# Kernel optimization log

Hardware: AMD Instinct MI355X
Metric: run time of the kernel (lower is better)

The kernel has to match this reference:

```python
import jax, jax.numpy as jnp
import numpy as np

GAMMA = 0.96875


def setup_inputs() -> dict:
    key = jax.random.key(0)
    kx, kq, kk, kv = jax.random.split(key, 4)
    B, T, D = 4, 2048, 1024
    x = jax.random.normal(kx, (B, T, D), dtype=jnp.float32)
    Wq = jax.random.normal(kq, (D, D), dtype=jnp.float32) * (1.0 / np.sqrt(D))
    Wk = jax.random.normal(kk, (D, D), dtype=jnp.float32) * (1.0 / np.sqrt(D))
    Wv = jax.random.normal(kv, (D, D), dtype=jnp.float32) * (1.0 / np.sqrt(D))
    return {"x": x, "Wq": Wq, "Wk": Wk, "Wv": Wv}


def reference(x, Wq, Wk, Wv):
    # x: [B, T, D_in]; projections are bias-free Dense layers
    B, T, _ = x.shape
    D = Wq.shape[1]
    Q = jnp.einsum("bti,id->btd", x, Wq)  # [B,T,D]
    K = jnp.einsum("bti,id->btd", x, Wk)
    V = jnp.einsum("bti,id->btd", x, Wv)

    gamma = jnp.asarray(GAMMA, x.dtype)

    # Original: s[t] = gamma*s[t-1] + K[:,t,:]^T @ V[:,t,:]   (a [D,D] state,
    # batch is CONTRACTED by the matmul), then only reduce_sum over the last
    # state axis is used. The recurrence is linear, so it collapses exactly to
    # a [D]-vector recurrence with m_t[d] = sum_b K[b,t,d] * (sum_e V[b,t,e]).
    m = jnp.einsum("btd,bt->td", K, V.sum(axis=-1))  # [T,D]

    def step(s, mt):
        s_new = gamma * s + mt
        return s_new, s_new

    # loop runs t = 1..T-1 starting from s = 0; afterwards s[0] = s[1]
    _, states = jax.lax.scan(step, jnp.zeros((D,), x.dtype), m[1:])  # [T-1,D]
    S = jnp.concatenate([states[:1], states], axis=0)  # [T,D]

    # tf.reshape([T,D] -> [-1, T]) is a row-major element scramble, then transpose
    S = S.reshape(-1, T).T  # [T,D] (scrambled, faithful to the original)

    return S[None, :, :] * Q  # broadcast over batch -> [B,T,D]
```

## Files before the change

### kernel.cpp

```cpp
#include <hip/hip_runtime.h>
#include <hip/hip_bf16.h>
#include <cstddef>

#define T_DIM 2048
#define D_DIM 1024
#define GAMMA_F 0.96875f

typedef __attribute__((ext_vector_type(8))) short bf16x8;
typedef __attribute__((ext_vector_type(4))) ushort ushortx4;
typedef __attribute__((ext_vector_type(8))) ushort ushortx8;
typedef __attribute__((ext_vector_type(4))) float f32x4;

#define AS1 __attribute__((address_space(1)))
#define AS3 __attribute__((address_space(3)))

static __device__ inline ushort f2bs(float f) {
    __hip_bfloat16 h = __float2bfloat16(f);
    return *reinterpret_cast<ushort*>(&h);
}

constexpr float gpw(int n) {
    float r = 1.f;
    for (int i = 0; i < n; ++i) r *= GAMMA_F;
    return r;
}

template <int N>
static __device__ __forceinline__ void vm_wait() {
    static_assert(N == 0 || N == 2 || N == 3 || N == 4 || N == 6 || N == 8,
                  "vm_wait<N>: N not in emitted set");
    if constexpr (N == 0)      asm volatile("s_waitcnt vmcnt(0)" ::: "memory");
    else if constexpr (N == 2) asm volatile("s_waitcnt vmcnt(2)" ::: "memory");
    else if constexpr (N == 3) asm volatile("s_waitcnt vmcnt(3)" ::: "memory");
    else if constexpr (N == 4) asm volatile("s_waitcnt vmcnt(4)" ::: "memory");
    else if constexpr (N == 6) asm volatile("s_waitcnt vmcnt(6)" ::: "memory");
    else if constexpr (N == 8) asm volatile("s_waitcnt vmcnt(8)" ::: "memory");
}
static __device__ __forceinline__ void raw_barrier() {
    asm volatile("s_barrier" ::: "memory");
}
static __device__ __forceinline__ void lgkm0() {
    asm volatile("s_waitcnt lgkmcnt(0)" ::: "memory");
}

__global__ __launch_bounds__(256) void k_prep(const float* __restrict__ Wk,
                                              const float* __restrict__ Wq,
                                              const float* __restrict__ Wv,
                                              ushort* __restrict__ WTk,
                                              ushort* __restrict__ WTq,
                                              float* __restrict__ wv_sum) {
    const int tid = threadIdx.x;
    if (blockIdx.z == 2) {
        __shared__ float red[4];
        const int i = blockIdx.y * 32 + blockIdx.x;
        const float* row = Wv + (size_t)i * D_DIM;
        float p = 0.f;
        for (int c = tid; c < D_DIM; c += 256) p += row[c];
        for (int o = 32; o; o >>= 1) p += __shfl_down(p, o);
        if ((tid & 63) == 0) red[tid >> 6] = p;
        __syncthreads();
        if (tid == 0) wv_sum[i] = red[0] + red[1] + red[2] + red[3];
        return;
    }
    const float* W = (blockIdx.z == 0) ? Wk : Wq;
    ushort* WT     = (blockIdx.z == 0) ? WTk : WTq;
    __shared__ float tile[32][33];
    const int tx = tid & 31, ty = tid >> 5;
    const int kb = blockIdx.x * 32, nb = blockIdx.y * 32;
    #pragma unroll
    for (int r = 0; r < 4; ++r)
        tile[ty + 8 * r][tx] = W[(size_t)(kb + ty + 8 * r) * 1024 + nb + tx];
    __syncthreads();
    #pragma unroll
    for (int r = 0; r < 4; ++r)
        WT[(size_t)(nb + ty + 8 * r) * 1024 + kb + tx] =
            f2bs(tile[tx][ty + 8 * r]);
}

__global__ __launch_bounds__(256) void k_vsum_y(const float* __restrict__ x,
                                                const float* __restrict__ wv_sum,
                                                ushort* __restrict__ yb,
                                                ushort* __restrict__ xb) {
    __shared__ float red[4][4];
    const int t = blockIdx.x;
    const int tid = threadIdx.x;
    const int lane = tid & 63, wv = tid >> 6;
    const int i0 = tid * 4;

    const float4 wvs = *(const float4*)(wv_sum + i0);

    float4 xv[4];
    #pragma unroll
    for (int b = 0; b < 4; ++b)
        xv[b] = *(const float4*)(x + ((size_t)b * T_DIM + t) * D_DIM + i0);

    #pragma unroll
    for (int b = 0; b < 4; ++b) {
        float p = xv[b].x * wvs.x + xv[b].y * wvs.y +
                  xv[b].z * wvs.z + xv[b].w * wvs.w;
        for (int o = 32; o; o >>= 1) p += __shfl_down(p, o);
        if (lane == 0) red[wv][b] = p;
    }
    __syncthreads();

    float vs[4];
    #pragma unroll
    for (int b = 0; b < 4; ++b)
        vs[b] = red[0][b] + red[1][b] + red[2][b] + red[3][b];

    #pragma unroll
    for (int b = 0; b < 4; ++b) {
        ushortx4 xw;
        xw[0] = f2bs(xv[b].x); xw[1] = f2bs(xv[b].y);
        xw[2] = f2bs(xv[b].z); xw[3] = f2bs(xv[b].w);
        *(ushortx4*)(xb + ((size_t)b * T_DIM + t) * D_DIM + i0) = xw;
    }

    ushortx4 yw;
    {
        float a0 = 0.f, a1 = 0.f, a2 = 0.f, a3 = 0.f;
        #pragma unroll
        for (int b = 0; b < 4; ++b) {
            a0 += xv[b].x * vs[b];
            a1 += xv[b].y * vs[b];
            a2 += xv[b].z * vs[b];
            a3 += xv[b].w * vs[b];
        }
        yw[0] = f2bs(a0); yw[1] = f2bs(a1); yw[2] = f2bs(a2); yw[3] = f2bs(a3);
    }
    *(ushortx4*)(yb + (size_t)t * D_DIM + i0) = yw;
}

template <int MF, int NF, int MODE>
__global__ __launch_bounds__(512, 4) void k_gemm(const ushort* __restrict__ A,
                                                 const ushort* __restrict__ BT,
                                                 float* __restrict__ C,
                                                 const float* __restrict__ S2,
                                                 float* __restrict__ tot) {
    static_assert(MODE != 0 || MF == 2, "fused scan1 requires 32-row wave tiles");
    constexpr int BM = 4 * MF * 16;
    constexpr int BN = 2 * NF * 16;
    constexpr int LOADS = BM / 64 + BN / 64;
    __shared__ ushort As[2][BM][64];
    __shared__ ushort Bs[2][BN][64];
    const int tid = threadIdx.x;
    const int lane = tid & 63, wid = tid >> 6;
    const int wr = wid >> 1, wc = wid & 1;
    const int rowBase = blockIdx.x * BM;
    const int colBase = blockIdx.y * BN;

    f32x4 acc[MF][NF];
    #pragma unroll
    for (int i = 0; i < MF; ++i)
        #pragma unroll
        for (int j = 0; j < NF; ++j) acc[i][j] = f32x4{0.f, 0.f, 0.f, 0.f};

    auto stage = [&](int buf, int kb) {
        #pragma unroll
        for (int q = 0; q < BM / 64; ++q) {
            const int s = q * 8192 + tid * 16;
            const int r = s >> 7, grp = (s >> 4) & 7;
            const int gcol = kb + (((grp ^ (r & 7)) & 7) << 3);
            __builtin_amdgcn_global_load_lds(
                (const AS1 void*)(A + (size_t)(rowBase + r) * 1024 + gcol),
                (AS3 void*)((AS3 char*)&As[buf][0][0] + s), 16, 0, 0);
        }
        #pragma unroll
        for (int q = 0; q < BN / 64; ++q) {
            const int s = q * 8192 + tid * 16;
            const int r = s >> 7, grp = (s >> 4) & 7;
            const int gcol = kb + (((grp ^ (r & 7)) & 7) << 3);
            __builtin_amdgcn_global_load_lds(
                (const AS1 void*)(BT + (size_t)(colBase + r) * 1024 + gcol),
                (AS3 void*)((AS3 char*)&Bs[buf][0][0] + s), 16, 0, 0);
        }
    };

    stage(0, 0);

    #pragma unroll 2
    for (int kt = 0; kt < 16; ++kt) {
        const int cur = kt & 1;
        if (kt < 15) {
            stage(cur ^ 1, (kt + 1) * 64);
            vm_wait<LOADS>();
        } else {
            vm_wait<0>();
        }
        raw_barrier();

        bf16x8 af[2][MF], bfv[2][NF];
        #pragma unroll
        for (int ks = 0; ks < 2; ++ks) {
            const int kg = ks * 4 + (lane >> 4);
            #pragma unroll
            for (int mi = 0; mi < MF; ++mi) {
                const int r = wr * (MF * 16) + mi * 16 + (lane & 15);
                af[ks][mi] = *(const bf16x8*)((const char*)&As[cur][0][0] +
                                              r * 128 + (((kg ^ (r & 7)) & 7) << 4));
            }
            #pragma unroll
            for (int ni = 0; ni < NF; ++ni) {
                const int r = wc * (NF * 16) + ni * 16 + (lane & 15);
                bfv[ks][ni] = *(const bf16x8*)((const char*)&Bs[cur][0][0] +
                                               r * 128 + (((kg ^ (r & 7)) & 7) << 4));
            }
        }
        #pragma unroll
        for (int ks = 0; ks < 2; ++ks)
            #pragma unroll
            for (int mi = 0; mi < MF; ++mi)
                #pragma unroll
                for (int ni = 0; ni < NF; ++ni)
                    acc[mi][ni] = __builtin_amdgcn_mfma_f32_16x16x32_bf16(
                        af[ks][mi], bfv[ks][ni], acc[mi][ni], 0, 0, 0);

        lgkm0();
        raw_barrier();
    }

    #pragma unroll
    for (int mi = 0; mi < MF; ++mi) {
        #pragma unroll
        for (int ni = 0; ni < NF; ++ni) {
            const int col = colBase + wc * (NF * 16) + ni * 16 + (lane & 15);
            #pragma unroll
            for (int q = 0; q < 4; ++q) {
                const int row = rowBase + wr * (MF * 16) + mi * 16 + (lane >> 4) * 4 + q;
                float v = acc[mi][ni][q];
                if (MODE == 1)
                    v *= S2[(size_t)(row & (T_DIM - 1)) * D_DIM + col];
                C[(size_t)row * D_DIM + col] = v;
            }
        }
    }

    if (MODE == 0) {
        const int h = lane >> 4;
        const int t3 = 3 - h;
        const float A0 = ((t3 & 1) ? gpw(4) : 1.f) * ((t3 & 2) ? gpw(8) : 1.f);
        const int chunk = blockIdx.x * 4 + wr;
        #pragma unroll
        for (int ni = 0; ni < NF; ++ni) {
            float part = 0.f;
            #pragma unroll
            for (int mi = 0; mi < MF; ++mi)
                #pragma unroll
                for (int q = 0; q < 4; ++q)
                    part += (A0 * gpw(16 * (MF - 1 - mi) + (3 - q))) * acc[mi][ni][q];
            if (chunk == 0 && h == 0)
                part -= (A0 * gpw(16 * (MF - 1) + 3)) * acc[0][ni][0];
            part += __shfl_xor(part, 16);
            part += __shfl_xor(part, 32);
            if (h == 0) {
                const int col = colBase + wc * (NF * 16) + ni * 16 + (lane & 15);
                tot[(size_t)chunk * D_DIM + col] = part;
            }
        }
    }
}

#define SC_L 32
#define SC_NC 64

__global__ __launch_bounds__(256) void k_scan2(const float* __restrict__ m,
                                               const float* __restrict__ tot,
                                               float* __restrict__ S2) {
    __shared__ float ls[128][65];
    const int tid = threadIdx.x;
    const int cl = tid & 63;
    const int ch = tid >> 6;
    const int col = blockIdx.x * 64 + cl;
    const int chg = blockIdx.y * 4 + ch;
    const int t0 = chg * SC_L;

    constexpr float gL = gpw(SC_L);

    float carry = 0.f, f = 1.f;
    for (int j = chg - 1; j >= 0; --j) {
        carry += f * tot[(size_t)j * D_DIM + col];
        f *= gL;
    }

    float r = carry, s1 = 0.f;
    #pragma unroll 4
    for (int k = 0; k < SC_L; ++k) {
        const int t = t0 + k;
        const float a = (t == 0) ? 0.f : m[(size_t)t * D_DIM + col];
        r = GAMMA_F * r + a;
        ls[ch * SC_L + k][cl] = r;
        if (t == 1) s1 = r;
    }
    if (blockIdx.y == 0 && ch == 0) ls[0][cl] = s1;
    __syncthreads();

    const int c0 = blockIdx.x * 64;
    const int tB = blockIdx.y * 128;
    for (int e = tid; e < 128 * 64; e += 256) {
        const int rr = e >> 6;
        const int j  = e & 63;
        const int hi = rr >> 6, cl2 = rr & 63;
        S2[(size_t)((hi << 10) + c0 + cl2) * D_DIM + (tB >> 1) + j] =
            ls[2 * j + hi][cl2];
    }
}

extern "C" void kernel_launch(void* const* d_in, const int* in_sizes, int n_in,
                              void* d_out, int out_size, void* d_ws, size_t ws_size,
                              hipStream_t stream) {
    const float* x  = (const float*)d_in[0];
    const float* Wq = (const float*)d_in[1];
    const float* Wk = (const float*)d_in[2];
    const float* Wv = (const float*)d_in[3];
    float* out = (float*)d_out;
    char* ws = (char*)d_ws;

    ushort* xb  = (ushort*)(ws);
    float*  m   = (float*)(ws + (16u << 20));
    ushort* yb  = (ushort*)(ws + (24u << 20));
    ushort* WTk = (ushort*)(ws + (28u << 20));
    ushort* WTq = (ushort*)(ws + (30u << 20));
    float*  S2  = (float*)(ws + (32u << 20));
    float*  tot = (float*)(ws + (40u << 20));
    float*  wv_sum = m;

    dim3 gP(32, 32, 3);
    k_prep<<<gP, 256, 0, stream>>>(Wk, Wq, Wv, WTk, WTq, wv_sum);

    k_vsum_y<<<T_DIM, 256, 0, stream>>>(x, wv_sum, (ushort*)yb, (ushort*)xb);

    dim3 gm(T_DIM / 128, D_DIM / 64);
    k_gemm<2, 2, 0><<<gm, 512, 0, stream>>>(yb, WTk, m, nullptr, tot);

    dim3 gs(D_DIM / 64, SC_NC / 4);
    k_scan2<<<gs, 256, 0, stream>>>(m, tot, S2);

    dim3 gq((4 * T_DIM) / 128, D_DIM / 128);
    k_gemm<2, 4, 1><<<gq, 512, 0, stream>>>(xb, WTq, out, S2, nullptr);
}
```

Baseline: 73.02 us.

## Rewrite Q projection GEMM with 32x32x16 MFMA and 4-wave 128x128 tiles

Splits the templated GEMM into a dedicated m-projection kernel and a new Q-projection kernel. The Q kernel uses 256 threads, 64x64 per-wave tiles built from 32x32x16 bf16 MFMA, and a K-step of 32 with XOR-swizzled LDS staging through global_load_lds. The goal is to cut LDS reads per FLOP and raise MFMA efficiency on the largest GEMM. In exchange it uses more accumulator registers and has a different epilogue write pattern, which may reduce occupancy or coalescing.

Measured after the change: 77.83 us. 1.07x slower.

```diff
diff --git a/kernel.cpp b/kernel.cpp
--- a/kernel.cpp
+++ b/kernel.cpp
@@ -10,6 +10,7 @@
 typedef __attribute__((ext_vector_type(4))) ushort ushortx4;
 typedef __attribute__((ext_vector_type(8))) ushort ushortx8;
 typedef __attribute__((ext_vector_type(4))) float f32x4;
+typedef __attribute__((ext_vector_type(16))) float f32x16;
 
 #define AS1 __attribute__((address_space(1)))
 #define AS3 __attribute__((address_space(3)))
@@ -131,13 +132,12 @@
     *(ushortx4*)(yb + (size_t)t * D_DIM + i0) = yw;
 }
 
-template <int MF, int NF, int MODE>
-__global__ __launch_bounds__(512, 4) void k_gemm(const ushort* __restrict__ A,
-                                                 const ushort* __restrict__ BT,
-                                                 float* __restrict__ C,
-                                                 const float* __restrict__ S2,
-                                                 float* __restrict__ tot) {
-    static_assert(MODE != 0 || MF == 2, "fused scan1 requires 32-row wave tiles");
+template <int MF, int NF>
+__global__ __launch_bounds__(512, 4) void k_gemm_m(const ushort* __restrict__ A,
+                                                   const ushort* __restrict__ BT,
+                                                   float* __restrict__ C,
+                                                   float* __restrict__ tot) {
+    static_assert(MF == 2, "fused scan1 requires 32-row wave tiles");
     constexpr int BM = 4 * MF * 16;
     constexpr int BN = 2 * NF * 16;
     constexpr int LOADS = BM / 64 + BN / 64;
@@ -227,15 +227,12 @@
             #pragma unroll
             for (int q = 0; q < 4; ++q) {
                 const int row = rowBase + wr * (MF * 16) + mi * 16 + (lane >> 4) * 4 + q;
-                float v = acc[mi][ni][q];
-                if (MODE == 1)
-                    v *= S2[(size_t)(row & (T_DIM - 1)) * D_DIM + col];
-                C[(size_t)row * D_DIM + col] = v;
-            }
-        }
-    }
-
-    if (MODE == 0) {
+                C[(size_t)row * D_DIM + col] = acc[mi][ni][q];
+            }
+        }
+    }
+
+    {
         const int h = lane >> 4;
         const int t3 = 3 - h;
         const float A0 = ((t3 & 1) ? gpw(4) : 1.f) * ((t3 & 2) ? gpw(8) : 1.f);
@@ -260,6 +257,107 @@
     }
 }
 
+__global__ __launch_bounds__(256, 4) void k_gemm_q(const ushort* __restrict__ A,
+                                                   const ushort* __restrict__ BT,
+                                                   float* __restrict__ C,
+                                                   const float* __restrict__ S2) {
+    __shared__ ushort As[2][128][32];
+    __shared__ ushort Bs[2][128][32];
+    const int tid = threadIdx.x;
+    const int lane = tid & 63, wid = tid >> 6;
+    const int wr = wid >> 1, wc = wid & 1;
+    const int rowBase = blockIdx.x * 128;
+    const int colBase = blockIdx.y * 128;
+
+    f32x16 acc[2][2];
+    #pragma unroll
+    for (int i = 0; i < 2; ++i)
+        #pragma unroll
+        for (int j = 0; j < 2; ++j)
+            #pragma unroll
+            for (int e = 0; e < 16; ++e) acc[i][j][e] = 0.f;
+
+    auto stage = [&](int buf, int kb) {
+        #pragma unroll
+        for (int q = 0; q < 2; ++q) {
+            const int s = q * 4096 + tid * 16;
+            const int r = s >> 6, g = (s >> 4) & 3;
+            const int gcol = kb + (((g ^ ((r >> 1) & 3)) & 3) << 3);
+            __builtin_amdgcn_global_load_lds(
+                (const AS1 void*)(A + (size_t)(rowBase + r) * 1024 + gcol),
+                (AS3 void*)((AS3 char*)&As[buf][0][0] + s), 16, 0, 0);
+        }
+        #pragma unroll
+        for (int q = 0; q < 2; ++q) {
+            const int s = q * 4096 + tid * 16;
+            const int r = s >> 6, g = (s >> 4) & 3;
+            const int gcol = kb + (((g ^ ((r >> 1) & 3)) & 3) << 3);
+            __builtin_amdgcn_global_load_lds(
+                (const AS1 void*)(BT + (size_t)(colBase + r) * 1024 + gcol),
+                (AS3 void*)((AS3 char*)&Bs[buf][0][0] + s), 16, 0, 0);
+        }
+    };
+
+    stage(0, 0);
+
+    #pragma unroll 2
+    for (int kt = 0; kt < 32; ++kt) {
+        const int cur = kt & 1;
+        if (kt < 31) {
+            stage(cur ^ 1, (kt + 1) * 32);
+            vm_wait<4>();
+        } else {
+            vm_wait<0>();
+        }
+        raw_barrier();
+
+        bf16x8 af[2][2], bfv[2][2];
+        #pragma unroll
+        for (int ks = 0; ks < 2; ++ks) {
+            const int g = ks * 2 + (lane >> 5);
+            #pragma unroll
+            for (int mi = 0; mi < 2; ++mi) {
+                const int r = wr * 64 + mi * 32 + (lane & 31);
+                af[ks][mi] = *(const bf16x8*)((const char*)&As[cur][0][0] +
+                                              r * 64 + (((g ^ ((r >> 1) & 3)) & 3) << 4));
+            }
+            #pragma unroll
+            for (int ni = 0; ni < 2; ++ni) {
+                const int r = wc * 64 + ni * 32 + (lane & 31);
+                bfv[ks][ni] = *(const bf16x8*)((const char*)&Bs[cur][0][0] +
+                                               r * 64 + (((g ^ ((r >> 1) & 3)) & 3) << 4));
+            }
+        }
+        #pragma unroll
+        for (int ks = 0; ks < 2; ++ks)
+            #pragma unroll
+            for (int mi = 0; mi < 2; ++mi)
+                #pragma unroll
+                for (int ni = 0; ni < 2; ++ni)
+                    acc[mi][ni] = __builtin_amdgcn_mfma_f32_32x32x16_bf16(
+                        af[ks][mi], bfv[ks][ni], acc[mi][ni], 0, 0, 0);
+
+        lgkm0();
+        raw_barrier();
+    }
+
+    #pragma unroll
+    for (int mi = 0; mi < 2; ++mi) {
+        #pragma unroll
+        for (int ni = 0; ni < 2; ++ni) {
+            const int col = colBase + wc * 64 + ni * 32 + (lane & 31);
+            #pragma unroll
+            for (int reg = 0; reg < 16; ++reg) {
+                const int row = rowBase + wr * 64 + mi * 32 +
+                                (reg & 3) + 8 * (reg >> 2) + 4 * (lane >> 5);
+                float v = acc[mi][ni][reg];
+                v *= S2[(size_t)(row & (T_DIM - 1)) * D_DIM + col];
+                C[(size_t)row * D_DIM + col] = v;
+            }
+        }
+    }
+}
+
 #define SC_L 32
 #define SC_NC 64
 
@@ -330,11 +428,11 @@
     k_vsum_y<<<T_DIM, 256, 0, stream>>>(x, wv_sum, (ushort*)yb, (ushort*)xb);
 
     dim3 gm(T_DIM / 128, D_DIM / 64);
-    k_gemm<2, 2, 0><<<gm, 512, 0, stream>>>(yb, WTk, m, nullptr, tot);
+    k_gemm_m<2, 2><<<gm, 512, 0, stream>>>(yb, WTk, m, tot);
 
     dim3 gs(D_DIM / 64, SC_NC / 4);
     k_scan2<<<gs, 256, 0, stream>>>(m, tot, S2);
 
     dim3 gq((4 * T_DIM) / 128, D_DIM / 128);
-    k_gemm<2, 4, 1><<<gq, 512, 0, stream>>>(xb, WTq, out, S2, nullptr);
-}
+    k_gemm_q<<<gq, 256, 0, stream>>>(xb, WTq, out, S2);
+}
```

## Fuse scan2 into the Q GEMM using a global semaphore

Applied to the files above, without the earlier changes.

Removes the separate scan kernel. Its work now runs in the first 256 blocks of the Q projection GEMM, which signal an atomic counter. Every GEMM block waits on that counter only before its epilogue, so the scan overlaps the Q matmul main loop and one launch is dropped. The wait assumes all 256 scan blocks are co-resident or already scheduled, which risks deadlock if they are not, and it adds a memset launch for the semaphore.

Result: slower. 108.0 us (+47.8%).

```diff
diff --git a/kernel.cpp b/kernel.cpp
--- a/kernel.cpp
+++ b/kernel.cpp
@@ -8,7 +8,6 @@
 
 typedef __attribute__((ext_vector_type(8))) short bf16x8;
 typedef __attribute__((ext_vector_type(4))) ushort ushortx4;
-typedef __attribute__((ext_vector_type(8))) ushort ushortx8;
 typedef __attribute__((ext_vector_type(4))) float f32x4;
 
 #define AS1 __attribute__((address_space(1)))
@@ -41,6 +40,22 @@
 }
 static __device__ __forceinline__ void lgkm0() {
     asm volatile("s_waitcnt lgkmcnt(0)" ::: "memory");
+}
+
+static __device__ __forceinline__ void sem_signal(unsigned* sem) {
+    __syncthreads();
+    if (threadIdx.x == 0) {
+        __threadfence();
+        atomicAdd(sem, 1u);
+    }
+}
+static __device__ __forceinline__ void sem_wait(unsigned* sem, unsigned target) {
+    if (threadIdx.x == 0) {
+        while (__hip_atomic_load(sem, __ATOMIC_RELAXED, __HIP_MEMORY_SCOPE_AGENT) < target)
+            __builtin_amdgcn_s_sleep(16);
+        __threadfence();
+    }
+    __syncthreads();
 }
 
 __global__ __launch_bounds__(256) void k_prep(const float* __restrict__ Wk,
@@ -131,12 +146,61 @@
     *(ushortx4*)(yb + (size_t)t * D_DIM + i0) = yw;
 }
 
+#define SC_L 32
+
+static __device__ __forceinline__ void scan2_body(char* smem, int bx, int by,
+                                                  const float* __restrict__ m,
+                                                  const float* __restrict__ tot,
+                                                  float* __restrict__ S2) {
+    float (*ls)[65] = (float(*)[65])smem;
+    const int tid = threadIdx.x;
+    if (tid < 256) {
+        const int cl = tid & 63;
+        const int ch = tid >> 6;
+        const int col = bx * 64 + cl;
+        const int chg = by * 4 + ch;
+        const int t0 = chg * SC_L;
+
+        constexpr float gL = gpw(SC_L);
+        float carry = 0.f, f = 1.f;
+        for (int j = chg - 1; j >= 0; --j) {
+            carry += f * tot[(size_t)j * D_DIM + col];
+            f *= gL;
+        }
+
+        float r = carry, s1 = 0.f;
+        #pragma unroll 4
+        for (int k = 0; k < SC_L; ++k) {
+            const int t = t0 + k;
+            const float a = (t == 0) ? 0.f : m[(size_t)t * D_DIM + col];
+            r = GAMMA_F * r + a;
+            ls[ch * SC_L + k][cl] = r;
+            if (t == 1) s1 = r;
+        }
+        if (by == 0 && ch == 0) ls[0][cl] = s1;
+    }
+    __syncthreads();
+
+    const int c0 = bx * 64;
+    const int tB = by * 128;
+    for (int e = tid; e < 128 * 64; e += 512) {
+        const int rr = e >> 6;
+        const int j  = e & 63;
+        const int hi = rr >> 6, cl2 = rr & 63;
+        S2[(size_t)((hi << 10) + c0 + cl2) * D_DIM + (tB >> 1) + j] =
+            ls[2 * j + hi][cl2];
+    }
+    __syncthreads();
+}
+
 template <int MF, int NF, int MODE>
 __global__ __launch_bounds__(512, 4) void k_gemm(const ushort* __restrict__ A,
                                                  const ushort* __restrict__ BT,
                                                  float* __restrict__ C,
-                                                 const float* __restrict__ S2,
-                                                 float* __restrict__ tot) {
+                                                 float* __restrict__ S2,
+                                                 float* __restrict__ tot,
+                                                 const float* __restrict__ m_in,
+                                                 unsigned* sem) {
     static_assert(MODE != 0 || MF == 2, "fused scan1 requires 32-row wave tiles");
     constexpr int BM = 4 * MF * 16;
     constexpr int BN = 2 * NF * 16;
@@ -149,6 +213,16 @@
     const int rowBase = blockIdx.x * BM;
     const int colBase = blockIdx.y * BN;
 
+    if (MODE == 1) {
+        const int lin = blockIdx.y * gridDim.x + blockIdx.x;
+        if (lin < 256) {
+            static_assert(MODE != 1 || sizeof(As) + sizeof(Bs) >= 128 * 65 * 4,
+                          "scan2 arena");
+            scan2_body((char*)&As[0][0][0], lin & 15, lin >> 4, m_in, tot, S2);
+            sem_signal(sem);
+        }
+    }
+
     f32x4 acc[MF][NF];
     #pragma unroll
     for (int i = 0; i < MF; ++i)
@@ -218,6 +292,8 @@
         lgkm0();
         raw_barrier();
     }
+
+    if (MODE == 1) sem_wait(sem, 256);
 
     #pragma unroll
     for (int mi = 0; mi < MF; ++mi) {
@@ -260,51 +336,6 @@
     }
 }
 
-#define SC_L 32
-#define SC_NC 64
-
-__global__ __launch_bounds__(256) void k_scan2(const float* __restrict__ m,
-                                               const float* __restrict__ tot,
-                                               float* __restrict__ S2) {
-    __shared__ float ls[128][65];
-    const int tid = threadIdx.x;
-    const int cl = tid & 63;
-    const int ch = tid >> 6;
-    const int col = blockIdx.x * 64 + cl;
-    const int chg = blockIdx.y * 4 + ch;
-    const int t0 = chg * SC_L;
-
-    constexpr float gL = gpw(SC_L);
-
-    float carry = 0.f, f = 1.f;
-    for (int j = chg - 1; j >= 0; --j) {
-        carry += f * tot[(size_t)j * D_DIM + col];
-        f *= gL;
-    }
-
-    float r = carry, s1 = 0.f;
-    #pragma unroll 4
-    for (int k = 0; k < SC_L; ++k) {
-        const int t = t0 + k;
-        const float a = (t == 0) ? 0.f : m[(size_t)t * D_DIM + col];
-        r = GAMMA_F * r + a;
-        ls[ch * SC_L + k][cl] = r;
-        if (t == 1) s1 = r;
-    }
-    if (blockIdx.y == 0 && ch == 0) ls[0][cl] = s1;
-    __syncthreads();
-
-    const int c0 = blockIdx.x * 64;
-    const int tB = blockIdx.y * 128;
-    for (int e = tid; e < 128 * 64; e += 256) {
-        const int rr = e >> 6;
-        const int j  = e & 63;
-        const int hi = rr >> 6, cl2 = rr & 63;
-        S2[(size_t)((hi << 10) + c0 + cl2) * D_DIM + (tB >> 1) + j] =
-            ls[2 * j + hi][cl2];
-    }
-}
-
 extern "C" void kernel_launch(void* const* d_in, const int* in_sizes, int n_in,
                               void* d_out, int out_size, void* d_ws, size_t ws_size,
                               hipStream_t stream) {
@@ -322,7 +353,10 @@
     ushort* WTq = (ushort*)(ws + (30u << 20));
     float*  S2  = (float*)(ws + (32u << 20));
     float*  tot = (float*)(ws + (40u << 20));
+    unsigned* sem = (unsigned*)(ws + (40u << 20) + (512u << 10));
     float*  wv_sum = m;
+
+    hipMemsetAsync(sem, 0, 256, stream);
 
     dim3 gP(32, 32, 3);
     k_prep<<<gP, 256, 0, stream>>>(Wk, Wq, Wv, WTk, WTq, wv_sum);
@@ -330,11 +364,9 @@
     k_vsum_y<<<T_DIM, 256, 0, stream>>>(x, wv_sum, (ushort*)yb, (ushort*)xb);
 
     dim3 gm(T_DIM / 128, D_DIM / 64);
-    k_gemm<2, 2, 0><<<gm, 512, 0, stream>>>(yb, WTk, m, nullptr, tot);
-
-    dim3 gs(D_DIM / 64, SC_NC / 4);
-    k_scan2<<<gs, 256, 0, stream>>>(m, tot, S2);
+    k_gemm<2, 2, 0><<<gm, 512, 0, stream>>>(yb, WTk, m, nullptr, tot,
+                                            nullptr, nullptr);
 
     dim3 gq((4 * T_DIM) / 128, D_DIM / 128);
-    k_gemm<2, 4, 1><<<gq, 512, 0, stream>>>(xb, WTq, out, S2, nullptr);
-}
+    k_gemm<2, 4, 1><<<gq, 512, 0, stream>>>(xb, WTq, out, S2, tot, m, sem);
+}
```
